# Optimization experiments

Measured on AMD Instinct MI355X. Metric: run time of the kernel, lower is better.

Reference implementation:

```python
import jax, jax.numpy as jnp
import numpy as np

# Static architecture dims (match init_kwargs)
B, T, NB, SX, SY = 1, 10, 10, 1200, 1200
ND, NS, DIV = 5, 5, 4            # dynamic bands, static bands, pool size
OX = OY = SX // DIV + 2          # 302 (conv pad1 -> pool floor -> conv pad1)
FLAT = NB * OX * OY              # 912040
PW = ((SX + 2) // DIV) * DIV     # 1200: maxpool floor-mode coverage of the 1202-wide map


def setup_inputs() -> dict:
    key = jax.random.key(0)
    ks = jax.random.split(key, 17)
    n = lambda k, s, sc=1.0: jax.random.normal(k, s, dtype=jnp.float32) * sc
    return {
        "x": n(ks[0], (B, T, NB, SX, SY)),
        "conv1_w": n(ks[1], (2 * NB, NB), 0.1),   # 1x1 conv as (out_c, in_c)
        "conv1_b": n(ks[2], (2 * NB,), 0.1),
        "conv2_w": n(ks[3], (NB, 2 * NB), 0.1),
        "conv2_b": n(ks[4], (NB,), 0.1),
        "w_ih": n(ks[5], (ND, 4), 0.5),           # per-band LSTM, gates i,f,g,o (H=1, in=1)
        "w_hh": n(ks[6], (ND, 4), 0.5),
        "b_ih": n(ks[7], (ND, 4), 0.5),
        "b_hh": n(ks[8], (ND, 4), 0.5),
        "fc1_w": n(ks[9], (64, FLAT), 0.001),
        "fc1_b": n(ks[10], (64,)),
        "fc2_w": n(ks[11], (64, 64), 0.1),
        "fc2_b": n(ks[12], (64,)),
        "fc3_w": n(ks[13], (16, 64), 0.1),
        "fc3_b": n(ks[14], (16,)),
        "fc4_w": n(ks[15], (3, 16), 0.1),
        "fc4_b": n(ks[16], (3,)),
    }


def _forward(x, conv1_w, conv1_b, conv2_w, conv2_b, w_ih, w_hh, b_ih, b_hh,
             fc1_w, fc1_b, fc2_w, fc2_b, fc3_w, fc3_b, fc4_w, fc4_b):
    xf = x.reshape(B * T, NB, SX, SY)
    # Conv2d(k=1, pad=1): zero-pad input ring then 1x1 conv + bias -> (BT, 2NB, 1202, 1202)
    xp = jnp.pad(xf, ((0, 0), (0, 0), (1, 1), (1, 1)))
    h = jnp.einsum('bcxy,oc->boxy', xp, conv1_w) + conv1_b[None, :, None, None]
    # MaxPool2d(k=4, s=4), floor mode: drop remainder cols/rows, reshape-max
    NW = PW // DIV  # 300
    h = h[:, :, :PW, :PW].reshape(B * T, 2 * NB, NW, DIV, NW, DIV).max(axis=(3, 5))
    # Second Conv2d(k=1, pad=1) -> (BT, NB, 302, 302)
    hp = jnp.pad(h, ((0, 0), (0, 0), (1, 1), (1, 1)))
    h = jnp.einsum('bcxy,oc->boxy', hp, conv2_w) + conv2_b[None, :, None, None]
    x5 = h.reshape(B, T, NB, OX, OY)
    dyn = x5[:, :, :ND]      # bandas_time = [0..4]
    stat = x5[:, -1, ND:]    # (B, NS, OX, OY)
    # Faithful to torch .view: raw row-major reinterpretation (B,T,ND,OX,OY) -> (B*OX*OY, T, ND)
    xd = dyn.reshape(B * OX * OY, T, ND)
    bias = (b_ih + b_hh)[None]  # (1, ND, 4)

    def step(carry, xt):
        hh, cc = carry  # each (PB, ND)
        g = xt[:, :, None] * w_ih[None] + hh[:, :, None] * w_hh[None] + bias
        i = jax.nn.sigmoid(g[..., 0])
        f = jax.nn.sigmoid(g[..., 1])
        gg = jnp.tanh(g[..., 2])
        o = jax.nn.sigmoid(g[..., 3])
        cc = f * cc + i * gg
        hh = o * jnp.tanh(cc)
        return (hh, cc), None

    z = jnp.zeros((B * OX * OY, ND), jnp.float32)
    (hT, _), _ = jax.lax.scan(step, (z, z), jnp.transpose(xd, (1, 0, 2)))
    x_dyn = hT.reshape(B, OX, OY, ND).transpose(0, 3, 1, 2)  # (B, ND, OX, OY)
    feat = jnp.concatenate([x_dyn, stat], axis=1).reshape(B, FLAT)
    y = feat @ fc1_w.T + fc1_b
    y = y @ fc2_w.T + fc2_b
    y = jax.nn.relu(y)
    y = y @ fc3_w.T + fc3_b
    y = y @ fc4_w.T + fc4_b
    return y


def reference(x, conv1_w, conv1_b, conv2_w, conv2_b, w_ih, w_hh, b_ih, b_hh,
              fc1_w, fc1_b, fc2_w, fc2_b, fc3_w, fc3_b, fc4_w, fc4_b):
    return _forward(x, conv1_w, conv1_b, conv2_w, conv2_b, w_ih, w_hh, b_ih, b_hh,
                    fc1_w, fc1_b, fc2_w, fc2_b, fc3_w, fc3_b, fc4_w, fc4_b)
```

## Files before the change

### kernel.cpp

```cpp
#include <hip/hip_runtime.h>
#include <math.h>

#define T_    10
#define NB_   10
#define C1_   20
#define SX_   1200
#define OX_   302
#define S2_   (OX_*OX_)
#define NP_   300
#define ND_   5
#define FLAT_ (NB_*S2_)
#define NBLK_FC1 512

typedef float f4 __attribute__((ext_vector_type(4), aligned(4)));

__global__ __launch_bounds__(256) void k_border(const float* __restrict__ b2,
                                                float* __restrict__ dynb,
                                                float* __restrict__ feat) {
    int s = blockIdx.x * 256 + threadIdx.x;
    if (s >= S2_) return;
    int ox = s / OX_, oy = s % OX_;
    if (ox != 0 && ox != OX_ - 1 && oy != 0 && oy != OX_ - 1) return;
#pragma unroll
    for (int d = 0; d < ND_; ++d) {
        float v = b2[d];
#pragma unroll
        for (int t = 0; t < T_; ++t) dynb[(t * ND_ + d) * S2_ + s] = v;
    }
#pragma unroll
    for (int c = 0; c < ND_; ++c) feat[(ND_ + c) * S2_ + s] = b2[ND_ + c];
}

__global__ __launch_bounds__(256) void k_convpool(const float* __restrict__ x,
                                                  const float* __restrict__ w1,
                                                  const float* __restrict__ b1,
                                                  const float* __restrict__ w2,
                                                  const float* __restrict__ b2,
                                                  float* __restrict__ dynb,
                                                  float* __restrict__ feat) {
    int py = blockIdx.x * 64 + threadIdx.x;
    int px = blockIdx.y * 4 + threadIdx.y;
    int t  = blockIdx.z;
    if (py >= NP_) return;

    float pool[C1_];
#pragma unroll
    for (int o = 0; o < C1_; ++o) pool[o] = -3.0e38f;

    int c0 = (py > 0) ? 4 * py - 1 : 0;
    int rs = (px > 0) ? 4 * px - 1 : 0;
    int re = 4 * px + 2;
    const float* xt = x + (size_t)t * NB_ * SX_ * SX_;

    for (int row = rs; row <= re; ++row) {
        f4 xv[NB_];
#pragma unroll
        for (int c = 0; c < NB_; ++c)
            xv[c] = *(const f4*)(xt + ((size_t)c * SX_ + row) * SX_ + c0);
#pragma unroll
        for (int o = 0; o < C1_; ++o) {
            float bb = b1[o];
            float h0 = bb, h1 = bb, h2 = bb, h3 = bb;
#pragma unroll
            for (int c = 0; c < NB_; ++c) {
                float w = w1[o * NB_ + c];
                h0 = fmaf(w, xv[c].x, h0);
                h1 = fmaf(w, xv[c].y, h1);
                h2 = fmaf(w, xv[c].z, h2);
                h3 = fmaf(w, xv[c].w, h3);
            }
            float m = fmaxf(fmaxf(h0, h1), h2);
            m = fmaxf(m, (py > 0) ? h3 : -3.0e38f);
            pool[o] = fmaxf(pool[o], m);
        }
    }
    if (px == 0 || py == 0) {
#pragma unroll
        for (int o = 0; o < C1_; ++o) pool[o] = fmaxf(pool[o], b1[o]);
    }

    int s = (px + 1) * OX_ + (py + 1);
    float out[NB_];
#pragma unroll
    for (int o2 = 0; o2 < NB_; ++o2) {
        float a = b2[o2];
#pragma unroll
        for (int o = 0; o < C1_; ++o) a = fmaf(w2[o2 * C1_ + o], pool[o], a);
        out[o2] = a;
    }
#pragma unroll
    for (int d = 0; d < ND_; ++d) dynb[(t * ND_ + d) * S2_ + s] = out[d];
    if (t == T_ - 1) {
#pragma unroll
        for (int c = 0; c < ND_; ++c) feat[(ND_ + c) * S2_ + s] = out[ND_ + c];
    }
}

__global__ __launch_bounds__(256) void k_lstm(const float* __restrict__ dynb,
                                              const float* __restrict__ w_ih,
                                              const float* __restrict__ w_hh,
                                              const float* __restrict__ b_ih,
                                              const float* __restrict__ b_hh,
                                              float* __restrict__ feat) {
    int i = blockIdx.x * 256 + threadIdx.x;
    if (i >= S2_ * ND_) return;
    int p = i / ND_, d = i - p * ND_;

    float wi[4], wh[4], bb[4];
#pragma unroll
    for (int g = 0; g < 4; ++g) {
        wi[g] = w_ih[d * 4 + g];
        wh[g] = w_hh[d * 4 + g];
        bb[g] = b_ih[d * 4 + g] + b_hh[d * 4 + g];
    }
    float h = 0.f, cc = 0.f;
    for (int tt = 0; tt < T_; ++tt) {
        float xt = dynb[p * (T_ * ND_) + tt * ND_ + d];
        float g0 = fmaf(xt, wi[0], fmaf(h, wh[0], bb[0]));
        float g1 = fmaf(xt, wi[1], fmaf(h, wh[1], bb[1]));
        float g2 = fmaf(xt, wi[2], fmaf(h, wh[2], bb[2]));
        float g3 = fmaf(xt, wi[3], fmaf(h, wh[3], bb[3]));
        float ig = 1.f / (1.f + expf(-g0));
        float fg = 1.f / (1.f + expf(-g1));
        float gg = tanhf(g2);
        float og = 1.f / (1.f + expf(-g3));
        cc = fg * cc + ig * gg;
        h  = og * tanhf(cc);
    }
    feat[d * S2_ + p] = h;
}

__global__ __launch_bounds__(256) void k_fc1(const float* __restrict__ feat,
                                             const float* __restrict__ w,
                                             float* __restrict__ partial) {
    __shared__ float red[4 * 64];
    int tid = threadIdx.x;
    float acc[64];
#pragma unroll
    for (int j = 0; j < 64; ++j) acc[j] = 0.f;
    const int NI4 = FLAT_ / 4;
    for (int i4 = blockIdx.x * 256 + tid; i4 < NI4; i4 += NBLK_FC1 * 256) {
        f4 f = *(const f4*)(feat + (size_t)i4 * 4);
#pragma unroll
        for (int j = 0; j < 64; ++j) {
            f4 wv = *(const f4*)(w + (size_t)j * FLAT_ + (size_t)i4 * 4);
            acc[j] = fmaf(wv.x, f.x, acc[j]);
            acc[j] = fmaf(wv.y, f.y, acc[j]);
            acc[j] = fmaf(wv.z, f.z, acc[j]);
            acc[j] = fmaf(wv.w, f.w, acc[j]);
        }
    }
    int lane = tid & 63, wid = tid >> 6;
#pragma unroll
    for (int j = 0; j < 64; ++j) {
        float v = acc[j];
#pragma unroll
        for (int off = 32; off >= 1; off >>= 1) v += __shfl_xor(v, off, 64);
        if (lane == 0) red[wid * 64 + j] = v;
    }
    __syncthreads();
    if (tid < 64) {
        float s = red[tid] + red[64 + tid] + red[128 + tid] + red[192 + tid];
        partial[blockIdx.x * 64 + tid] = s;
    }
}

__global__ __launch_bounds__(256) void k_head(const float* __restrict__ partial,
                                              const float* __restrict__ fc1_b,
                                              const float* __restrict__ fc2_w,
                                              const float* __restrict__ fc2_b,
                                              const float* __restrict__ fc3_w,
                                              const float* __restrict__ fc3_b,
                                              const float* __restrict__ fc4_w,
                                              const float* __restrict__ fc4_b,
                                              float* __restrict__ out) {
    __shared__ float r4[256];
    __shared__ float y1[64], y2[64], y3[16];
    int tid = threadIdx.x;
    int j = tid & 63, q = tid >> 6;
    float s = 0.f;
    for (int b = q; b < NBLK_FC1; b += 4) s += partial[b * 64 + j];
    r4[tid] = s;
    __syncthreads();
    if (tid < 64)
        y1[tid] = r4[tid] + r4[64 + tid] + r4[128 + tid] + r4[192 + tid] + fc1_b[tid];
    __syncthreads();
    if (tid < 64) {
        float a = fc2_b[tid];
#pragma unroll
        for (int k = 0; k < 64; ++k) a = fmaf(fc2_w[tid * 64 + k], y1[k], a);
        y2[tid] = fmaxf(a, 0.f);
    }
    __syncthreads();
    if (tid < 16) {
        float a = fc3_b[tid];
#pragma unroll
        for (int k = 0; k < 64; ++k) a = fmaf(fc3_w[tid * 64 + k], y2[k], a);
        y3[tid] = a;
    }
    __syncthreads();
    if (tid < 3) {
        float a = fc4_b[tid];
#pragma unroll
        for (int k = 0; k < 16; ++k) a = fmaf(fc4_w[tid * 16 + k], y3[k], a);
        out[tid] = a;
    }
}

extern "C" void kernel_launch(void* const* d_in, const int* in_sizes, int n_in,
                              void* d_out, int out_size, void* d_ws, size_t ws_size,
                              hipStream_t stream) {
    const float* x     = (const float*)d_in[0];
    const float* w1    = (const float*)d_in[1];
    const float* b1    = (const float*)d_in[2];
    const float* w2    = (const float*)d_in[3];
    const float* b2    = (const float*)d_in[4];
    const float* w_ih  = (const float*)d_in[5];
    const float* w_hh  = (const float*)d_in[6];
    const float* b_ih  = (const float*)d_in[7];
    const float* b_hh  = (const float*)d_in[8];
    const float* fc1_w = (const float*)d_in[9];
    const float* fc1_b = (const float*)d_in[10];
    const float* fc2_w = (const float*)d_in[11];
    const float* fc2_b = (const float*)d_in[12];
    const float* fc3_w = (const float*)d_in[13];
    const float* fc3_b = (const float*)d_in[14];
    const float* fc4_w = (const float*)d_in[15];
    const float* fc4_b = (const float*)d_in[16];

    float* ws      = (float*)d_ws;
    float* dynb    = ws;
    float* feat    = ws + (size_t)T_ * ND_ * S2_;
    float* partial = feat + FLAT_;

    hipLaunchKernelGGL(k_border, dim3((S2_ + 255) / 256), dim3(256), 0, stream,
                       b2, dynb, feat);
    hipLaunchKernelGGL(k_convpool, dim3(5, 75, T_), dim3(64, 4), 0, stream,
                       x, w1, b1, w2, b2, dynb, feat);
    hipLaunchKernelGGL(k_lstm, dim3((S2_ * ND_ + 255) / 256), dim3(256), 0, stream,
                       dynb, w_ih, w_hh, b_ih, b_hh, feat);
    hipLaunchKernelGGL(k_fc1, dim3(NBLK_FC1), dim3(256), 0, stream,
                       feat, fc1_w, partial);
    hipLaunchKernelGGL(k_head, dim3(1), dim3(256), 0, stream,
                       partial, fc1_b, fc2_w, fc2_b, fc3_w, fc3_b, fc4_w, fc4_b,
                       (float*)d_out);
}
```

Measured before the change: 254.0 us.

## Align convpool loads via lane shuffle and split fc1 outputs across two blocks

The conv-pool kernel now has each lane load an aligned 4-wide chunk starting at a multiple of 4. The pooling window (which is offset by one column) is rebuilt by combining this lane's last column with the neighbour lane's first three columns via __shfl_down, so each block of 64 lanes produces 63 outputs. The f4 typedef drops aligned(4), allowing full 16-byte vector loads. The fc1 kernel splits its 64 output rows into two blockIdx.y halves, halving per-thread accumulators to raise occupancy, at the cost of reading the feature vector twice.

```diff
diff --git a/kernel.cpp b/kernel.cpp
--- a/kernel.cpp
+++ b/kernel.cpp
@@ -12,7 +12,7 @@
 #define FLAT_ (NB_*S2_)
 #define NBLK_FC1 512
 
-typedef float f4 __attribute__((ext_vector_type(4), aligned(4)));
+typedef float f4 __attribute__((ext_vector_type(4)));
 
 __global__ __launch_bounds__(256) void k_border(const float* __restrict__ b2,
                                                 float* __restrict__ dynb,
@@ -38,25 +38,28 @@
                                                   const float* __restrict__ b2,
                                                   float* __restrict__ dynb,
                                                   float* __restrict__ feat) {
-    int py = blockIdx.x * 64 + threadIdx.x;
-    int px = blockIdx.y * 4 + threadIdx.y;
-    int t  = blockIdx.z;
-    if (py >= NP_) return;
-
-    float pool[C1_];
-#pragma unroll
-    for (int o = 0; o < C1_; ++o) pool[o] = -3.0e38f;
-
-    int c0 = (py > 0) ? 4 * py - 1 : 0;
-    int rs = (px > 0) ? 4 * px - 1 : 0;
-    int re = 4 * px + 2;
+    const int lane  = threadIdx.x;
+    const int obase = blockIdx.x * 63;
+    const int px    = blockIdx.y * 4 + threadIdx.y;
+    const int t     = blockIdx.z;
+
+    const int lc  = 4 * (obase - 1 + lane);
+    const int lcc = lc < 0 ? 0 : (lc > SX_ - 4 ? SX_ - 4 : lc);
+    const bool m3valid = (lc >= 0);
+
+    float pool012[C1_], pool3[C1_];
+#pragma unroll
+    for (int o = 0; o < C1_; ++o) { pool012[o] = -3.0e38f; pool3[o] = -3.0e38f; }
+
+    const int rs = (px > 0) ? 4 * px - 1 : 0;
+    const int re = 4 * px + 2;
     const float* xt = x + (size_t)t * NB_ * SX_ * SX_;
 
     for (int row = rs; row <= re; ++row) {
         f4 xv[NB_];
 #pragma unroll
         for (int c = 0; c < NB_; ++c)
-            xv[c] = *(const f4*)(xt + ((size_t)c * SX_ + row) * SX_ + c0);
+            xv[c] = *(const f4*)(xt + ((size_t)c * SX_ + row) * SX_ + lcc);
 #pragma unroll
         for (int o = 0; o < C1_; ++o) {
             float bb = b1[o];
@@ -69,30 +72,39 @@
                 h2 = fmaf(w, xv[c].z, h2);
                 h3 = fmaf(w, xv[c].w, h3);
             }
-            float m = fmaxf(fmaxf(h0, h1), h2);
-            m = fmaxf(m, (py > 0) ? h3 : -3.0e38f);
-            pool[o] = fmaxf(pool[o], m);
-        }
-    }
-    if (px == 0 || py == 0) {
-#pragma unroll
-        for (int o = 0; o < C1_; ++o) pool[o] = fmaxf(pool[o], b1[o]);
-    }
-
-    int s = (px + 1) * OX_ + (py + 1);
-    float out[NB_];
-#pragma unroll
-    for (int o2 = 0; o2 < NB_; ++o2) {
-        float a = b2[o2];
-#pragma unroll
-        for (int o = 0; o < C1_; ++o) a = fmaf(w2[o2 * C1_ + o], pool[o], a);
-        out[o2] = a;
-    }
-#pragma unroll
-    for (int d = 0; d < ND_; ++d) dynb[(t * ND_ + d) * S2_ + s] = out[d];
-    if (t == T_ - 1) {
-#pragma unroll
-        for (int c = 0; c < ND_; ++c) feat[(ND_ + c) * S2_ + s] = out[ND_ + c];
+            pool012[o] = fmaxf(pool012[o], fmaxf(fmaxf(h0, h1), h2));
+            pool3[o]   = fmaxf(pool3[o], h3);
+        }
+    }
+
+    const int py = obase + lane;
+    const bool edge = (px == 0) | (py == 0);
+    float pool[C1_];
+#pragma unroll
+    for (int o = 0; o < C1_; ++o) {
+        float m3    = m3valid ? pool3[o] : -3.0e38f;
+        float other = __shfl_down(pool012[o], 1, 64);
+        float p = fmaxf(m3, other);
+        if (edge) p = fmaxf(p, b1[o]);
+        pool[o] = p;
+    }
+
+    if (lane < 63 && py < NP_) {
+        int s = (px + 1) * OX_ + (py + 1);
+        float out[NB_];
+#pragma unroll
+        for (int o2 = 0; o2 < NB_; ++o2) {
+            float a = b2[o2];
+#pragma unroll
+            for (int o = 0; o < C1_; ++o) a = fmaf(w2[o2 * C1_ + o], pool[o], a);
+            out[o2] = a;
+        }
+#pragma unroll
+        for (int d = 0; d < ND_; ++d) dynb[(t * ND_ + d) * S2_ + s] = out[d];
+        if (t == T_ - 1) {
+#pragma unroll
+            for (int c = 0; c < ND_; ++c) feat[(ND_ + c) * S2_ + s] = out[ND_ + c];
+        }
     }
 }
 
@@ -133,17 +145,19 @@
 __global__ __launch_bounds__(256) void k_fc1(const float* __restrict__ feat,
                                              const float* __restrict__ w,
                                              float* __restrict__ partial) {
-    __shared__ float red[4 * 64];
+    __shared__ float red[4][32];
     int tid = threadIdx.x;
-    float acc[64];
-#pragma unroll
-    for (int j = 0; j < 64; ++j) acc[j] = 0.f;
+    int jbase = blockIdx.y * 32;
+    float acc[32];
+#pragma unroll
+    for (int j = 0; j < 32; ++j) acc[j] = 0.f;
     const int NI4 = FLAT_ / 4;
+    const float* wb = w + (size_t)jbase * FLAT_;
     for (int i4 = blockIdx.x * 256 + tid; i4 < NI4; i4 += NBLK_FC1 * 256) {
         f4 f = *(const f4*)(feat + (size_t)i4 * 4);
 #pragma unroll
-        for (int j = 0; j < 64; ++j) {
-            f4 wv = *(const f4*)(w + (size_t)j * FLAT_ + (size_t)i4 * 4);
+        for (int j = 0; j < 32; ++j) {
+            f4 wv = *(const f4*)(wb + (size_t)j * FLAT_ + (size_t)i4 * 4);
             acc[j] = fmaf(wv.x, f.x, acc[j]);
             acc[j] = fmaf(wv.y, f.y, acc[j]);
             acc[j] = fmaf(wv.z, f.z, acc[j]);
@@ -152,16 +166,16 @@
     }
     int lane = tid & 63, wid = tid >> 6;
 #pragma unroll
-    for (int j = 0; j < 64; ++j) {
+    for (int j = 0; j < 32; ++j) {
         float v = acc[j];
 #pragma unroll
         for (int off = 32; off >= 1; off >>= 1) v += __shfl_xor(v, off, 64);
-        if (lane == 0) red[wid * 64 + j] = v;
-    }
-    __syncthreads();
-    if (tid < 64) {
-        float s = red[tid] + red[64 + tid] + red[128 + tid] + red[192 + tid];
-        partial[blockIdx.x * 64 + tid] = s;
+        if (lane == 0) red[wid][j] = v;
+    }
+    __syncthreads();
+    if (tid < 32) {
+        float s = red[0][tid] + red[1][tid] + red[2][tid] + red[3][tid];
+        partial[blockIdx.x * 64 + jbase + tid] = s;
     }
 }
 
@@ -239,7 +253,7 @@
                        x, w1, b1, w2, b2, dynb, feat);
     hipLaunchKernelGGL(k_lstm, dim3((S2_ * ND_ + 255) / 256), dim3(256), 0, stream,
                        dynb, w_ih, w_hh, b_ih, b_hh, feat);
-    hipLaunchKernelGGL(k_fc1, dim3(NBLK_FC1), dim3(256), 0, stream,
+    hipLaunchKernelGGL(k_fc1, dim3(NBLK_FC1, 2), dim3(256), 0, stream,
                        feat, fc1_w, partial);
     hipLaunchKernelGGL(k_head, dim3(1), dim3(256), 0, stream,
                        partial, fc1_b, fc2_w, fc2_b, fc3_w, fc3_b, fc4_w, fc4_b,
```

After: 242.9 us. 1.05x faster.
